# Kernel optimization log

Measured on AMD Instinct MI355X. Metric: run time of the kernel, lower is better.

Reference implementation:

```python
import jax, jax.numpy as jnp
import numpy as np

EMBED = 256
HEADS = 8
HD = EMBED // HEADS
LEVELS = 4
POINTS = 4
FFN_H = 1024
BS = 8
LQ = 900
SHAPES = [(100, 100), (50, 50), (25, 25), (13, 13)]


def setup_inputs() -> dict:
    key = jax.random.key(0)
    ks = jax.random.split(key, 20)
    nv = sum(h * w for h, w in SHAPES)
    starts = np.cumsum([0] + [h * w for h, w in SHAPES])[:-1]
    inp = {
        "queries": jax.random.normal(ks[0], (BS, LQ, EMBED), jnp.float32),
        "memory": jax.random.normal(ks[1], (BS, nv, EMBED), jnp.float32),
        "query_pos": jax.random.normal(ks[2], (BS, LQ, EMBED), jnp.float32),
        "reference_points": jax.random.uniform(ks[3], (BS, LQ, LEVELS, 4), jnp.float32) * 0.9 + 0.05,
        "spatial_shapes": jnp.asarray(SHAPES, jnp.int32),
        "level_start_index": jnp.asarray(starts, jnp.int32),
    }
    def lin(k, din, dout):
        k1, k2 = jax.random.split(k)
        w = jax.random.normal(k1, (din, dout), jnp.float32) * 0.02
        b = jax.random.normal(k2, (dout,), jnp.float32) * 0.01
        return w, b
    specs = [("Wq", "bq", EMBED, EMBED), ("Wk", "bk", EMBED, EMBED), ("Wv", "bv", EMBED, EMBED),
             ("Wo", "bo", EMBED, EMBED), ("Wvd", "bvd", EMBED, EMBED),
             ("Woff", "boff", EMBED, HEADS * LEVELS * POINTS * 2),
             ("Watt", "batt", EMBED, HEADS * LEVELS * POINTS),
             ("Wop", "bop", EMBED, EMBED), ("Wg", "bg", 2 * EMBED, 2 * EMBED),
             ("W1", "b1", EMBED, FFN_H), ("W2", "b2", FFN_H, EMBED)]
    for i, (wn, bn, di, do) in enumerate(specs):
        w, b = lin(ks[4 + i], di, do)
        inp[wn] = w
        inp[bn] = b
    for n in ["ln1", "ln2", "ln3"]:
        inp[n + "_s"] = jnp.ones((EMBED,), jnp.float32)
        inp[n + "_b"] = jnp.zeros((EMBED,), jnp.float32)
    return inp


def _ln(x, s, b):
    m = jnp.mean(x, -1, keepdims=True)
    v = jnp.mean(jnp.square(x - m), -1, keepdims=True)
    return (x - m) * jax.lax.rsqrt(v + 1e-5) * s + b


def _bilinear(v_l, lx, ly, H, W):
    # v_l: [bs,h,H*W,hd]; lx,ly: [bs,h,lq,p] normalized in [0,1]
    # grid_sample(align_corners=False, padding=zeros) semantics
    px = lx * W - 0.5
    py = ly * H - 0.5
    x0 = jnp.floor(px)
    y0 = jnp.floor(py)
    wx = px - x0
    wy = py - y0
    x0i = x0.astype(jnp.int32)
    y0i = y0.astype(jnp.int32)
    bs, h, lq, p = lx.shape
    out = jnp.zeros((bs, h, lq, p, HD), v_l.dtype)
    for dy in (0, 1):
        for dx in (0, 1):
            xi = x0i + dx
            yi = y0i + dy
            w = (wx if dx else 1.0 - wx) * (wy if dy else 1.0 - wy)
            valid = (xi >= 0) & (xi < W) & (yi >= 0) & (yi < H)
            idx = jnp.clip(yi, 0, H - 1) * W + jnp.clip(xi, 0, W - 1)
            g = jnp.take_along_axis(v_l, idx.reshape(bs, h, lq * p)[..., None], axis=2)
            g = g.reshape(bs, h, lq, p, HD)
            out = out + w[..., None] * jnp.where(valid[..., None], g, 0.0)
    return out


def reference(queries, memory, query_pos, reference_points, spatial_shapes, level_start_index,
              Wq, bq, Wk, bk, Wv, bv, Wo, bo, Wvd, bvd, Woff, boff, Watt, batt, Wop, bop,
              Wg, bg, W1, b1, W2, b2, ln1_s, ln1_b, ln2_s, ln2_b, ln3_s, ln3_b):
    bs, lq, _ = queries.shape
    shp = np.asarray(spatial_shapes)
    st = np.asarray(level_start_index)

    # ---- self attention (pre-norm, q=k=x+pos, v=x) ----
    x = _ln(queries, ln1_s, ln1_b)
    qk = x + query_pos
    Q = (qk @ Wq + bq).reshape(bs, lq, HEADS, HD)
    K = (qk @ Wk + bk).reshape(bs, lq, HEADS, HD)
    V = (x @ Wv + bv).reshape(bs, lq, HEADS, HD)
    scores = jnp.einsum('bqhd,bkhd->bhqk', Q, K) * (1.0 / np.sqrt(HD))
    attn = jax.nn.softmax(scores, axis=-1)
    sa = jnp.einsum('bhqk,bkhd->bqhd', attn, V).reshape(bs, lq, EMBED) @ Wo + bo
    x1 = queries + sa  # dropout is identity in eval

    # ---- MS-deformable cross attention ----
    y = _ln(x1, ln2_s, ln2_b)
    qc = y + query_pos
    val = (memory @ Wvd + bvd).reshape(bs, -1, HEADS, HD).transpose(0, 2, 1, 3)  # [bs,h,Nv,hd]
    off = (qc @ Woff + boff).reshape(bs, lq, HEADS, LEVELS, POINTS, 2)
    aw = jax.nn.softmax((qc @ Watt + batt).reshape(bs, lq, HEADS, LEVELS * POINTS), axis=-1)
    aw = aw.reshape(bs, lq, HEADS, LEVELS, POINTS)
    rp = reference_points[:, :, None, :, None, :]  # [bs,lq,1,L,1,4]
    loc = rp[..., :2] + off / POINTS * rp[..., 2:] * 0.5  # [bs,lq,h,L,p,2]

    out = jnp.zeros((bs, HEADS, lq, HD), queries.dtype)
    for l in range(LEVELS):
        H, W = int(shp[l, 0]), int(shp[l, 1])
        s0 = int(st[l])
        v_l = val[:, :, s0:s0 + H * W]
        lx = jnp.transpose(loc[:, :, :, l, :, 0], (0, 2, 1, 3))  # [bs,h,lq,p]
        ly = jnp.transpose(loc[:, :, :, l, :, 1], (0, 2, 1, 3))
        samp = _bilinear(v_l, lx, ly, H, W)  # [bs,h,lq,p,hd]
        w = jnp.transpose(aw[:, :, :, l], (0, 2, 1, 3))  # [bs,h,lq,p]
        out = out + jnp.sum(w[..., None] * samp, axis=3)
    cross = out.transpose(0, 2, 1, 3).reshape(bs, lq, EMBED) @ Wop + bop

    # ---- gated fusion ----
    gi = jnp.concatenate([x1, cross], axis=-1)
    g = jax.nn.sigmoid(gi @ Wg + bg)
    x2 = g[..., :EMBED] * x1 + g[..., EMBED:] * cross

    # ---- FFN ----
    z = _ln(x2, ln3_s, ln3_b)
    ffn = jax.nn.relu(z @ W1 + b1) @ W2 + b2
    return (x2 + ffn, aw, loc)
```

## Files before the change

kernel.cpp:

```cpp
#include <hip/hip_runtime.h>
#include <hip/hip_bf16.h>
#include <math.h>

#define BB 8
#define LQ 900
#define EE 256
#define NH 8
#define HD 32
#define NL 4
#define NP 4
#define FFN_H 1024

typedef __bf16 bf16x8 __attribute__((ext_vector_type(8)));
typedef float f32x4 __attribute__((ext_vector_type(4)));
typedef unsigned short u16x8 __attribute__((ext_vector_type(8)));

__device__ __forceinline__ unsigned short f2b(float f) {
    union { float f; unsigned int u; } v; v.f = f;
    unsigned int u = v.u;
    unsigned int r = (u + 0x7fffu + ((u >> 16) & 1u)) >> 16;
    return (unsigned short)r;
}
__device__ __forceinline__ float b2f(unsigned short h) {
    union { unsigned int u; float f; } v; v.u = ((unsigned int)h) << 16; return v.f;
}

typedef __attribute__((address_space(3))) unsigned int* lds_ptr_t;
typedef const __attribute__((address_space(1))) unsigned int* gbl_ptr_t;
#define GLOAD16(g, l) __builtin_amdgcn_global_load_lds((gbl_ptr_t)(g), (lds_ptr_t)(l), 16, 0, 0)
#define VMCNT(n) asm volatile("s_waitcnt vmcnt(" #n ")" ::: "memory")
#define LGKM0()  asm volatile("s_waitcnt lgkmcnt(0)" ::: "memory")

struct TDesc { const float* src; unsigned short* dst; int K, N, tile0; };
struct TPack {
    TDesc d[11];
    const float *bq, *bk, *boff, *batt;
    float *bqk, *boa;
};

__global__ __launch_bounds__(256) void prep_kernel(
    TPack p,
    const float* __restrict__ queries, const float* __restrict__ qpos,
    const float* __restrict__ ln1_s, const float* __restrict__ ln1_b,
    unsigned short* __restrict__ x_b, unsigned short* __restrict__ qk_b)
{
    const int bi = blockIdx.x;
    const int t = threadIdx.x;

    if (bi < 1248) {
        int di = 0;
#pragma unroll
        for (int i = 1; i < 11; ++i) if (bi >= p.d[i].tile0) di = i;
        TDesc d = p.d[di];
        int tt = bi - d.tile0;
        int tn = (d.N + 31) >> 5;
        int tk = tt / tn, tc = tt % tn;
        __shared__ float tile[32][33];
        int tx = t & 31, ty = t >> 5;
#pragma unroll
        for (int i = 0; i < 4; ++i) {
            int kk = tk * 32 + ty + i * 8, nn = tc * 32 + tx;
            tile[ty + i * 8][tx] = d.src[(size_t)kk * d.N + nn];
        }
        __syncthreads();
#pragma unroll
        for (int i = 0; i < 4; ++i) {
            int nn = tc * 32 + ty + i * 8, kk = tk * 32 + tx;
            d.dst[(size_t)nn * d.K + kk] = f2b(tile[tx][ty + i * 8]);
        }
        return;
    }
    if (bi < 1252) {
        int which = bi - 1248;
        if (which == 0)      p.bqk[t] = p.bq[t];
        else if (which == 1) p.bqk[256 + t] = p.bk[t];
        else if (which == 2) p.boa[t] = p.boff[t];
        else if (t < 128)    p.boa[256 + t] = p.batt[t];
        return;
    }
    {
        const int row = bi - 1252;
        const int w = t >> 6, lane = t & 63;
        __shared__ float red[4];
        float v = queries[(size_t)row * EE + t];
        float sum = v;
#pragma unroll
        for (int o = 32; o; o >>= 1) sum += __shfl_xor(sum, o, 64);
        if (lane == 0) red[w] = sum;
        __syncthreads();
        float mean = (red[0] + red[1] + red[2] + red[3]) * (1.0f / 256.0f);
        __syncthreads();
        float dd = v - mean;
        float sq = dd * dd;
#pragma unroll
        for (int o = 32; o; o >>= 1) sq += __shfl_xor(sq, o, 64);
        if (lane == 0) red[w] = sq;
        __syncthreads();
        float var = (red[0] + red[1] + red[2] + red[3]) * (1.0f / 256.0f);
        float y = dd * rsqrtf(var + 1e-5f) * ln1_s[t] + ln1_b[t];
        x_b[(size_t)row * EE + t]  = f2b(y);
        qk_b[(size_t)row * EE + t] = f2b(y + qpos[(size_t)row * EE + t]);
    }
}

struct GD {
    const unsigned short* A;
    const float* Af;
    const unsigned short* Bt;
    const float* bias;
    const float* resid;
    float* outF;
    unsigned short* outB;
    const float* lnS; const float* lnB; const float* lnAdd;
    unsigned short* lnOut;
    int M, K, N, ntN, tile0, ldOutB, outBoff, act, aF32;
};
struct GB { GD d[3]; int nd, tot; };

template<int BN>
__global__ __launch_bounds__(256, (BN == 128) ? 4 : 2) void gemm_pipe(GB g) {
    __shared__ __align__(16) unsigned short ldsb[2][(64 + BN) * 32];
    __shared__ float lnred[2][64][2];
    const int tid = threadIdx.x;
    const int l = tid & 63, w = tid >> 6;
    const int wr = w >> 1, wc = w & 1;
    constexpr int NJ = BN / 32;

    int t = blockIdx.x;
    if (t >= g.tot) return;
    int d = 0;
    while (d + 1 < g.nd && t >= g.d[d + 1].tile0) ++d;

    const int sc = tid & 3;
    float4 fA[2];

    auto stage = [&](int dd, int tt, int ks, int pp) {
        const GD& D = g.d[dd];
        int local = tt - D.tile0;
        int m0 = (local / D.ntN) * 64;
        int n0 = (local % D.ntN) * BN;
        unsigned short* base = &ldsb[pp][0];
        if (D.aF32) {
            int row = tid >> 2;
            int rg = m0 + row; int mm = D.M - 1; rg = rg < mm ? rg : mm;
            int ck = (sc ^ ((row >> 1) & 3)) * 8;
            const float* src = D.Af + (size_t)rg * D.K + (ks << 5) + ck;
            fA[0] = *(const float4*)src;
            fA[1] = *(const float4*)(src + 4);
        } else {
            int row = w * 16 + (l >> 2);
            int rg = m0 + row; int mm = D.M - 1; rg = rg < mm ? rg : mm;
            int schunk = ((l & 3) ^ ((row >> 1) & 3)) << 4;
            GLOAD16((const char*)(D.A + (size_t)rg * D.K + (ks << 5)) + schunk,
                    base + (w * 16) * 32);
        }
#pragma unroll
        for (int ib = 0; ib < BN / 64; ++ib) {
            int row = ib * 64 + w * 16 + (l >> 2);
            int rg = n0 + row; int nn = D.N - 1; rg = rg < nn ? rg : nn;
            int schunk = ((l & 3) ^ ((row >> 1) & 3)) << 4;
            GLOAD16((const char*)(D.Bt + (size_t)rg * D.K + (ks << 5)) + schunk,
                    base + 2048 + (ib * 64 + w * 16) * 32);
        }
    };
    auto commitA = [&](int pp) {
        int row = tid >> 2;
        u16x8 o;
        o[0] = f2b(fA[0].x); o[1] = f2b(fA[0].y); o[2] = f2b(fA[0].z); o[3] = f2b(fA[0].w);
        o[4] = f2b(fA[1].x); o[5] = f2b(fA[1].y); o[6] = f2b(fA[1].z); o[7] = f2b(fA[1].w);
        *(u16x8*)((char*)&ldsb[pp][0] + row * 64 + sc * 16) = o;
    };

    stage(d, t, 0, 0);
    if (g.d[d].aF32) { commitA(0); LGKM0(); }
    int p = 0;

    while (true) {
        const GD D = g.d[d];
        int local = t - D.tile0;
        const int m0 = (local / D.ntN) * 64;
        const int n0 = (local % D.ntN) * BN;
        const int nk = D.K >> 5;

        f32x4 acc[2][NJ];
#pragma unroll
        for (int i = 0; i < 2; ++i)
#pragma unroll
            for (int j = 0; j < NJ; ++j) acc[i][j] = (f32x4){0.f, 0.f, 0.f, 0.f};

        for (int ks = 0; ks < nk; ++ks) {
            int nt = t, nks = ks + 1, ndd = d;
            bool have = true;
            if (nks == nk) {
                nt = t + gridDim.x; nks = 0;
                if (nt >= g.tot) have = false;
                else { while (ndd + 1 < g.nd && nt >= g.d[ndd + 1].tile0) ++ndd; }
            }
            bool stagedAF = have && g.d[ndd].aF32;
            if (have) {
                stage(ndd, nt, nks, p ^ 1);
                if (stagedAF) {
                    if constexpr (BN == 128) { VMCNT(4); } else { VMCNT(6); }
                } else {
                    if constexpr (BN == 128) { VMCNT(3); } else { VMCNT(5); }
                }
            } else {
                VMCNT(0);
            }
            __builtin_amdgcn_sched_barrier(0);
            __builtin_amdgcn_s_barrier();
            __builtin_amdgcn_sched_barrier(0);
            {
                const char* base = (const char*)&ldsb[p][0];
                const int rch = ((l >> 4) ^ ((l >> 1) & 3)) << 4;
                bf16x8 af[2];
#pragma unroll
                for (int i = 0; i < 2; ++i) {
                    int row = wr * 32 + i * 16 + (l & 15);
                    af[i] = *(const bf16x8*)(base + row * 64 + rch);
                }
#pragma unroll
                for (int j = 0; j < NJ; ++j) {
                    int row = wc * (BN / 2) + j * 16 + (l & 15);
                    bf16x8 bfr = *(const bf16x8*)(base + 4096 + row * 64 + rch);
#pragma unroll
                    for (int i = 0; i < 2; ++i)
                        acc[i][j] = __builtin_amdgcn_mfma_f32_16x16x32_bf16(af[i], bfr, acc[i][j], 0, 0, 0);
                }
            }
            if (stagedAF) { commitA(p ^ 1); LGKM0(); }
            __builtin_amdgcn_sched_barrier(0);
            __builtin_amdgcn_s_barrier();
            __builtin_amdgcn_sched_barrier(0);
            p ^= 1;
        }

#pragma unroll
        for (int i = 0; i < 2; ++i) {
#pragma unroll
            for (int r = 0; r < 4; ++r) {
                int gm = m0 + wr * 32 + i * 16 + ((l >> 4) << 2) + r;
                if (gm >= D.M) continue;
#pragma unroll
                for (int j = 0; j < NJ; ++j) {
                    int gn = n0 + wc * (BN / 2) + j * 16 + (l & 15);
                    if (gn >= D.N) continue;
                    float v = acc[i][j][r];
                    if (D.bias)  v += D.bias[gn];
                    if (D.resid) v += D.resid[(size_t)gm * D.N + gn];
                    if (D.act == 1)      v = fmaxf(v, 0.f);
                    else if (D.act == 2) v = 1.0f / (1.0f + __expf(-v));
                    acc[i][j][r] = v;
                    if (D.outF) D.outF[(size_t)gm * D.N + gn] = v;
                    if (D.outB) D.outB[(size_t)gm * D.ldOutB + D.outBoff + gn] = f2b(v);
                }
            }
        }

        if constexpr (BN == 256) {
            if (D.lnOut) {
#pragma unroll
                for (int i = 0; i < 2; ++i) {
#pragma unroll
                    for (int r = 0; r < 4; ++r) {
                        float s1 = 0.f, s2 = 0.f;
#pragma unroll
                        for (int j = 0; j < NJ; ++j) {
                            float v = acc[i][j][r];
                            s1 += v; s2 += v * v;
                        }
#pragma unroll
                        for (int o = 1; o <= 8; o <<= 1) {
                            s1 += __shfl_xor(s1, o, 64);
                            s2 += __shfl_xor(s2, o, 64);
                        }
                        if ((l & 15) == 0) {
                            int row = wr * 32 + i * 16 + ((l >> 4) << 2) + r;
                            lnred[wc][row][0] = s1;
                            lnred[wc][row][1] = s2;
                        }
                    }
                }
                __syncthreads();
#pragma unroll
                for (int i = 0; i < 2; ++i) {
#pragma unroll
                    for (int r = 0; r < 4; ++r) {
                        int row = wr * 32 + i * 16 + ((l >> 4) << 2) + r;
                        int gm = m0 + row;
                        if (gm >= D.M) continue;
                        float mean = (lnred[0][row][0] + lnred[1][row][0]) * (1.0f / 256.0f);
                        float msq  = (lnred[0][row][1] + lnred[1][row][1]) * (1.0f / 256.0f);
                        float rs = rsqrtf(msq - mean * mean + 1e-5f);
#pragma unroll
                        for (int j = 0; j < NJ; ++j) {
                            int gn = wc * (BN / 2) + j * 16 + (l & 15);
                            float y = (acc[i][j][r] - mean) * rs * D.lnS[gn] + D.lnB[gn]
                                      + D.lnAdd[(size_t)gm * 256 + gn];
                            D.lnOut[(size_t)gm * 256 + gn] = f2b(y);
                        }
                    }
                }
            }
        }

        t += gridDim.x;
        if (t >= g.tot) break;
        while (d + 1 < g.nd && t >= g.d[d + 1].tile0) ++d;
    }
}

__global__ __launch_bounds__(256) void attn_mfma(
    const unsigned short* __restrict__ QK, const unsigned short* __restrict__ Vb,
    unsigned short* __restrict__ outB)
{
    const int qt = blockIdx.x;
    const int bh = blockIdx.y;
    const int b = bh >> 3, h = bh & 7;
    const int tid = threadIdx.x;
    const int w = tid >> 6, l = tid & 63;

    __shared__ __align__(16) unsigned short Ks[64 * 32];
    __shared__ __align__(16) unsigned short VT[32 * 64];
    __shared__ __align__(16) unsigned short Ps[4][64 * 20];

    const int qrow_w = qt * 64 + w * 16;
    int qr = qrow_w + (l & 15); qr = qr < LQ ? qr : LQ - 1;
    bf16x8 qf = *(const bf16x8*)(QK + ((size_t)(b * LQ + qr)) * 512 + h * 32 + (l >> 4) * 8);

    f32x4 acc0 = {0.f, 0.f, 0.f, 0.f}, acc1 = {0.f, 0.f, 0.f, 0.f};
    float m_run = -1e30f, l_run = 0.f;
    const float scale = 0.17677669529663689f;
    const f32x4 z4 = {0.f, 0.f, 0.f, 0.f};

    const int key = tid >> 2;
    const int dg = (tid & 3) * 8;
    u16x8 kvc, vvc, kvn, vvn;
    {
        int krow = key; krow = krow < LQ ? krow : LQ - 1;
        size_t base = (size_t)(b * LQ + krow);
        kvc = *(const u16x8*)(QK + base * 512 + 256 + h * 32 + dg);
        vvc = *(const u16x8*)(Vb + base * 256 + h * 32 + dg);
    }

    for (int kt = 0; kt < 15; ++kt) {
        __syncthreads();
        *(u16x8*)((char*)Ks + key * 64 + ((dg * 2) ^ ((key & 3) << 4))) = kvc;
#pragma unroll
        for (int e = 0; e < 8; ++e) {
            int dd = dg + e;
            *(unsigned short*)((char*)VT + dd * 128 + ((key * 2) ^ ((dd & 7) << 4))) = vvc[e];
        }
        if (kt < 14) {
            int krow = (kt + 1) * 64 + key; krow = krow < LQ ? krow : LQ - 1;
            size_t base = (size_t)(b * LQ + krow);
            kvn = *(const u16x8*)(QK + base * 512 + 256 + h * 32 + dg);
            vvn = *(const u16x8*)(Vb + base * 256 + h * 32 + dg);
        }
        __syncthreads();

        float p[4][4];
        float tmax = -1e30f;
#pragma unroll
        for (int m = 0; m < 4; ++m) {
            int kr = m * 16 + (l & 15);
            bf16x8 kf = *(const bf16x8*)((const char*)Ks + kr * 64 +
                        (((l >> 4) * 16) ^ ((kr & 3) << 4)));
            f32x4 sf = __builtin_amdgcn_mfma_f32_16x16x32_bf16(kf, qf, z4, 0, 0, 0);
#pragma unroll
            for (int r = 0; r < 4; ++r) {
                int kk = kt * 64 + m * 16 + (l >> 4) * 4 + r;
                float sv = (kk < LQ) ? sf[r] * scale : -1e30f;
                p[m][r] = sv;
                tmax = fmaxf(tmax, sv);
            }
        }
        tmax = fmaxf(tmax, __shfl_xor(tmax, 16, 64));
        tmax = fmaxf(tmax, __shfl_xor(tmax, 32, 64));
        float newm = fmaxf(m_run, tmax);
        float corr = __expf(m_run - newm);
        m_run = newm;
        float tsum = 0.f;
#pragma unroll
        for (int m = 0; m < 4; ++m)
#pragma unroll
            for (int r = 0; r < 4; ++r) {
                float e = __expf(p[m][r] - newm);
                p[m][r] = e;
                tsum += e;
            }
        tsum += __shfl_xor(tsum, 16, 64);
        tsum += __shfl_xor(tsum, 32, 64);
        l_run = l_run * corr + tsum;
        acc0 *= corr;
        acc1 *= corr;

        unsigned short* pw = &Ps[w][0];
#pragma unroll
        for (int m = 0; m < 4; ++m)
#pragma unroll
            for (int r = 0; r < 4; ++r) {
                int kk = m * 16 + (l >> 4) * 4 + r;
                pw[kk * 20 + (l & 15)] = f2b(p[m][r]);
            }

#pragma unroll
        for (int s = 0; s < 2; ++s) {
            union { unsigned short u[8]; bf16x8 v; } pb;
#pragma unroll
            for (int j = 0; j < 8; ++j)
                pb.u[j] = pw[(s * 32 + (l >> 4) * 8 + j) * 20 + (l & 15)];
#pragma unroll
            for (int m2 = 0; m2 < 2; ++m2) {
                int dd = m2 * 16 + (l & 15);
                bf16x8 vf = *(const bf16x8*)((const char*)VT + dd * 128 +
                            ((s * 64 + (l >> 4) * 16) ^ ((dd & 7) << 4)));
                if (m2 == 0) acc0 = __builtin_amdgcn_mfma_f32_16x16x32_bf16(vf, pb.v, acc0, 0, 0, 0);
                else         acc1 = __builtin_amdgcn_mfma_f32_16x16x32_bf16(vf, pb.v, acc1, 0, 0, 0);
            }
        }
        if (kt < 14) { kvc = kvn; vvc = vvn; }
    }

    float inv = 1.0f / l_run;
    int q = qrow_w + (l & 15);
    if (q < LQ) {
        size_t obase = ((size_t)(b * LQ + q)) * 256 + h * 32;
#pragma unroll
        for (int r = 0; r < 4; ++r) {
            int d0 = (l >> 4) * 4 + r;
            outB[obase + d0]      = f2b(acc0[r] * inv);
            outB[obase + 16 + d0] = f2b(acc1[r] * inv);
        }
    }
}

__global__ __launch_bounds__(256) void sample_fused(
    const float* __restrict__ off_att, const float* __restrict__ refp,
    const unsigned short* __restrict__ val,
    const int* __restrict__ shapes, const int* __restrict__ starts,
    float* __restrict__ aw_out, float* __restrict__ loc_out,
    unsigned short* __restrict__ samp, int NV)
{
    const int row = blockIdx.x;
    const int b = row / LQ;
    const int t = threadIdx.x;
    const int h = t >> 5, d = t & 31;

    __shared__ float l_logit[128];
    __shared__ float l_aw[128];
    __shared__ float l_loc[256];
    __shared__ int l_sh[NL * 2];
    __shared__ int l_st[NL];

    if (t < 128) l_logit[t] = off_att[(size_t)row * 384 + 256 + t];
    {
        float o = off_att[(size_t)row * 384 + t];
        int c = t & 1;
        int lv = (t >> 3) & 3;
        float rc = refp[((size_t)row * 4 + lv) * 4 + c];
        float rs = refp[((size_t)row * 4 + lv) * 4 + 2 + c];
        float loc = rc + o * 0.125f * rs;
        l_loc[t] = loc;
        loc_out[(size_t)row * 256 + t] = loc;
    }
    if (t < NL * 2) l_sh[t] = shapes[t];
    if (t < NL) l_st[t] = starts[t];
    __syncthreads();
    if (t < 128) {
        int hh = t >> 4;
        float mx = -1e30f;
#pragma unroll
        for (int i = 0; i < 16; ++i) mx = fmaxf(mx, l_logit[hh * 16 + i]);
        float sum = 0.f;
#pragma unroll
        for (int i = 0; i < 16; ++i) sum += __expf(l_logit[hh * 16 + i] - mx);
        float aw = __expf(l_logit[t] - mx) / sum;
        l_aw[t] = aw;
        aw_out[(size_t)row * 128 + t] = aw;
    }
    __syncthreads();

    float acc = 0.f;
    const unsigned short* vb = val + (size_t)b * NV * EE + h * HD + d;

#pragma unroll
    for (int lv = 0; lv < NL; ++lv) {
        const int Hh = l_sh[lv * 2], Ww = l_sh[lv * 2 + 1];
        const int s0 = l_st[lv];
#pragma unroll
        for (int p = 0; p < NP; ++p) {
            const int base = ((h * NL + lv) * NP + p) * 2;
            float lx = l_loc[base], ly = l_loc[base + 1];
            float wgt0 = l_aw[h * 16 + lv * NP + p];
            float px = lx * (float)Ww - 0.5f;
            float py = ly * (float)Hh - 0.5f;
            float x0f = floorf(px), y0f = floorf(py);
            float wx = px - x0f, wy = py - y0f;
            int x0 = (int)x0f, y0 = (int)y0f;
#pragma unroll
            for (int dy = 0; dy < 2; ++dy) {
                int yi = y0 + dy;
                bool vy = (yi >= 0) && (yi < Hh);
                int yc = min(max(yi, 0), Hh - 1);
                float wyv = dy ? wy : 1.f - wy;
#pragma unroll
                for (int dx = 0; dx < 2; ++dx) {
                    int xi = x0 + dx;
                    bool vv = vy && (xi >= 0) && (xi < Ww);
                    int xc = min(max(xi, 0), Ww - 1);
                    float wgt = wgt0 * wyv * (dx ? wx : 1.f - wx);
                    float gv = b2f(vb[(size_t)(s0 + yc * Ww + xc) * EE]);
                    acc += vv ? wgt * gv : 0.f;
                }
            }
        }
    }
    samp[(size_t)row * EE + t] = f2b(acc);
}

__global__ __launch_bounds__(256) void gate_ln3(
    const float* __restrict__ g, const float* __restrict__ x1,
    const float* __restrict__ cross, const float* __restrict__ s,
    const float* __restrict__ bln, float* __restrict__ x2out,
    unsigned short* __restrict__ zb)
{
    const int row = blockIdx.x;
    const int t = threadIdx.x;
    const int w = t >> 6;
    const int lane = t & 63;
    __shared__ float red[4];

    float g1 = g[(size_t)row * 512 + t];
    float g2 = g[(size_t)row * 512 + 256 + t];
    float v = g1 * x1[(size_t)row * EE + t] + g2 * cross[(size_t)row * EE + t];
    x2out[(size_t)row * EE + t] = v;

    float sum = v;
#pragma unroll
    for (int o = 32; o; o >>= 1) sum += __shfl_xor(sum, o, 64);
    if (lane == 0) red[w] = sum;
    __syncthreads();
    float mean = (red[0] + red[1] + red[2] + red[3]) * (1.0f / 256.0f);
    __syncthreads();

    float d = v - mean;
    float sq = d * d;
#pragma unroll
    for (int o = 32; o; o >>= 1) sq += __shfl_xor(sq, o, 64);
    if (lane == 0) red[w] = sq;
    __syncthreads();
    float var = (red[0] + red[1] + red[2] + red[3]) * (1.0f / 256.0f);

    float y = d * rsqrtf(var + 1e-5f) * s[t] + bln[t];
    zb[(size_t)row * EE + t] = f2b(y);
}

extern "C" void kernel_launch(void* const* d_in, const int* in_sizes, int n_in,
                              void* d_out, int out_size, void* d_ws, size_t ws_size,
                              hipStream_t stream)
{
    const float* queries   = (const float*)d_in[0];
    const float* memory    = (const float*)d_in[1];
    const float* query_pos = (const float*)d_in[2];
    const float* refp      = (const float*)d_in[3];
    const int*   shapes    = (const int*)d_in[4];
    const int*   starts    = (const int*)d_in[5];
    const float* Wq  = (const float*)d_in[6],  *bq  = (const float*)d_in[7];
    const float* Wk  = (const float*)d_in[8],  *bk  = (const float*)d_in[9];
    const float* Wv  = (const float*)d_in[10], *bv  = (const float*)d_in[11];
    const float* Wo  = (const float*)d_in[12], *bo  = (const float*)d_in[13];
    const float* Wvd = (const float*)d_in[14], *bvd = (const float*)d_in[15];
    const float* Woff= (const float*)d_in[16], *boff= (const float*)d_in[17];
    const float* Watt= (const float*)d_in[18], *batt= (const float*)d_in[19];
    const float* Wop = (const float*)d_in[20], *bop = (const float*)d_in[21];
    const float* Wg  = (const float*)d_in[22], *bg  = (const float*)d_in[23];
    const float* W1  = (const float*)d_in[24], *b1  = (const float*)d_in[25];
    const float* W2  = (const float*)d_in[26], *b2  = (const float*)d_in[27];
    const float* ln1_s = (const float*)d_in[28], *ln1_b = (const float*)d_in[29];
    const float* ln2_s = (const float*)d_in[30], *ln2_b = (const float*)d_in[31];
    const float* ln3_s = (const float*)d_in[32], *ln3_b = (const float*)d_in[33];

    const int NV = in_sizes[1] / (BB * EE);
    const int Mq = BB * LQ;
    const int Mv = BB * NV;
    const long memN = (long)Mv * EE;

    char* W8 = (char*)d_ws;
    size_t off = 0;
    auto alloc = [&](size_t bytes) { char* p = W8 + off; off += (bytes + 255) & ~(size_t)255; return p; };

    unsigned short* val_b = (unsigned short*)alloc((size_t)memN * 2);
    unsigned short* WtQK  = (unsigned short*)alloc(512 * 256 * 2);
    unsigned short* WtV   = (unsigned short*)alloc(256 * 256 * 2);
    unsigned short* WtO   = (unsigned short*)alloc(256 * 256 * 2);
    unsigned short* WtVD  = (unsigned short*)alloc(256 * 256 * 2);
    unsigned short* WtOA  = (unsigned short*)alloc(384 * 256 * 2);
    unsigned short* WtOP  = (unsigned short*)alloc(256 * 256 * 2);
    unsigned short* WtG   = (unsigned short*)alloc(512 * 512 * 2);
    unsigned short* Wt1   = (unsigned short*)alloc(1024 * 256 * 2);
    unsigned short* Wt2   = (unsigned short*)alloc(256 * 1024 * 2);
    float*          bqk   = (float*)alloc(512 * 4);
    float*          boa   = (float*)alloc(384 * 4);
    unsigned short* qkb   = (unsigned short*)alloc((size_t)Mq * 512 * 2);
    unsigned short* vb_buf= (unsigned short*)alloc((size_t)Mq * 256 * 2);
    unsigned short* av_buf= (unsigned short*)alloc((size_t)Mq * 256 * 2);
    float*          x1    = (float*)alloc((size_t)Mq * 256 * 4);
    unsigned short* xc_cat= (unsigned short*)alloc((size_t)Mq * 512 * 2);
    unsigned short* qc_b  = (unsigned short*)alloc((size_t)Mq * 256 * 2);
    unsigned short* qk_b  = (unsigned short*)alloc((size_t)Mq * 256 * 2);
    float*          cross = (float*)alloc((size_t)Mq * 256 * 4);

    unsigned short* x_b = (unsigned short*)cross;
    float* off_att = (float*)qkb;
    unsigned short* samp_b = av_buf;
    float* gbuf = (float*)val_b;
    float* x2   = (float*)((char*)val_b + (size_t)Mq * 512 * 4);
    unsigned short* z_b = (unsigned short*)((char*)x2 + (size_t)Mq * 256 * 4);
    unsigned short* hidden_b = (unsigned short*)((char*)z_b + (size_t)Mq * 256 * 2);

    float* out0    = (float*)d_out;
    float* aw_out  = out0 + (size_t)Mq * 256;
    float* loc_out = aw_out + (size_t)Mq * 128;

    dim3 blk(256);
    const int tMq = (Mq + 63) / 64;
    const int tv  = (Mv + 63) / 64;

    TPack tp;
    tp.d[0]  = { Wq,   WtQK,             256, 256,    0 };
    tp.d[1]  = { Wk,   WtQK + 256 * 256, 256, 256,   64 };
    tp.d[2]  = { Wv,   WtV,              256, 256,  128 };
    tp.d[3]  = { Wo,   WtO,              256, 256,  192 };
    tp.d[4]  = { Wvd,  WtVD,             256, 256,  256 };
    tp.d[5]  = { Woff, WtOA,             256, 256,  320 };
    tp.d[6]  = { Watt, WtOA + 256 * 256, 256, 128,  384 };
    tp.d[7]  = { Wop,  WtOP,             256, 256,  416 };
    tp.d[8]  = { Wg,   WtG,              512, 512,  480 };
    tp.d[9]  = { W1,   Wt1,              256, 1024, 736 };
    tp.d[10] = { W2,   Wt2,             1024, 256,  992 };
    tp.bq = bq; tp.bk = bk; tp.boff = boff; tp.batt = batt;
    tp.bqk = bqk; tp.boa = boa;
    prep_kernel<<<1252 + Mq, blk, 0, stream>>>(
        tp, queries, query_pos, ln1_s, ln1_b, x_b, qk_b);

    {
        GB g; g.nd = 3;
        g.d[0] = { nullptr, memory, WtVD, bvd, nullptr, nullptr, val_b,
                   nullptr, nullptr, nullptr, nullptr,
                   Mv, 256, 256, 2, 0, 256, 0, 0, 1 };
        g.d[1] = { qk_b, nullptr, WtQK, bqk, nullptr, nullptr, qkb,
                   nullptr, nullptr, nullptr, nullptr,
                   Mq, 256, 512, 4, tv * 2, 512, 0, 0, 0 };
        g.d[2] = { x_b, nullptr, WtV, bv, nullptr, nullptr, vb_buf,
                   nullptr, nullptr, nullptr, nullptr,
                   Mq, 256, 256, 2, tv * 2 + tMq * 4, 256, 0, 0, 0 };
        g.tot = tv * 2 + tMq * 6;
        gemm_pipe<128><<<1536, blk, 0, stream>>>(g);
    }

    attn_mfma<<<dim3(15, BB * NH), blk, 0, stream>>>(qkb, vb_buf, av_buf);

    {
        GB g; g.nd = 1;
        g.d[0] = { av_buf, nullptr, WtO, bo, queries, x1, xc_cat,
                   ln2_s, ln2_b, query_pos, qc_b,
                   Mq, 256, 256, 1, 0, 512, 0, 0, 0 };
        g.tot = tMq;
        gemm_pipe<256><<<tMq, blk, 0, stream>>>(g);
    }

    {
        GB g; g.nd = 1;
        g.d[0] = { qc_b, nullptr, WtOA, boa, nullptr, off_att, nullptr,
                   nullptr, nullptr, nullptr, nullptr,
                   Mq, 256, 384, 3, 0, 384, 0, 0, 0 };
        g.tot = tMq * 3;
        gemm_pipe<128><<<g.tot, blk, 0, stream>>>(g);
    }

    sample_fused<<<Mq, blk, 0, stream>>>(off_att, refp, val_b, shapes, starts,
                                         aw_out, loc_out, samp_b, NV);

    {
        GB g; g.nd = 1;
        g.d[0] = { samp_b, nullptr, WtOP, bop, nullptr, cross, xc_cat,
                   nullptr, nullptr, nullptr, nullptr,
                   Mq, 256, 256, 2, 0, 512, 256, 0, 0 };
        g.tot = tMq * 2;
        gemm_pipe<128><<<g.tot, blk, 0, stream>>>(g);
    }

    {
        GB g; g.nd = 1;
        g.d[0] = { xc_cat, nullptr, WtG, bg, nullptr, gbuf, nullptr,
                   nullptr, nullptr, nullptr, nullptr,
                   Mq, 512, 512, 4, 0, 512, 0, 2, 0 };
        g.tot = tMq * 4;
        gemm_pipe<128><<<g.tot, blk, 0, stream>>>(g);
    }

    gate_ln3<<<Mq, blk, 0, stream>>>(gbuf, x1, cross, ln3_s, ln3_b, x2, z_b);

    {
        GB g; g.nd = 1;
        g.d[0] = { z_b, nullptr, Wt1, b1, nullptr, nullptr, hidden_b,
                   nullptr, nullptr, nullptr, nullptr,
                   Mq, 256, 1024, 8, 0, 1024, 0, 1, 0 };
        g.tot = tMq * 8;
        gemm_pipe<128><<<g.tot, blk, 0, stream>>>(g);
    }

    {
        GB g; g.nd = 1;
        g.d[0] = { hidden_b, nullptr, Wt2, b2, x2, out0, nullptr,
                   nullptr, nullptr, nullptr, nullptr,
                   Mq, 1024, 256, 2, 0, 256, 0, 0, 0 };
        g.tot = tMq * 2;
        gemm_pipe<128><<<g.tot, blk, 0, stream>>>(g);
    }
}
```

Baseline: 333.5 us.

## Fold Wop into gate weights and batch cross/gate GEMMs; pre-convert memory to bf16

Folds the output projection Wop into the second half of the gate weight matrix (Wop·Wg_bottom, plus a folded bias), so the gate GEMM can consume the sampled features directly. The cross projection and the gate GEMM then run in a single batched launch instead of two dependent launches. Memory is also converted to bf16 inside the prep kernel so the value-projection GEMM uses the async LDS load path instead of fp32 loads with per-tile conversion. In exchange, prep gains a naive 256-long dot loop per weight column and an extra full pass over memory, and the folded weights are rounded to bf16 after the product, which slightly changes numerics.

```diff
diff --git a/kernel.cpp b/kernel.cpp
--- a/kernel.cpp
+++ b/kernel.cpp
@@ -33,24 +33,28 @@
 
 struct TDesc { const float* src; unsigned short* dst; int K, N, tile0; };
 struct TPack {
-    TDesc d[11];
+    TDesc d[10];
     const float *bq, *bk, *boff, *batt;
     float *bqk, *boa;
+    const float *Wg_src, *Wop_src, *bop_src, *bg_src;
+    unsigned short* WtGF;
+    float* bgg;
 };
 
 __global__ __launch_bounds__(256) void prep_kernel(
     TPack p,
     const float* __restrict__ queries, const float* __restrict__ qpos,
     const float* __restrict__ ln1_s, const float* __restrict__ ln1_b,
-    unsigned short* __restrict__ x_b, unsigned short* __restrict__ qk_b)
+    unsigned short* __restrict__ x_b, unsigned short* __restrict__ qk_b,
+    const float* __restrict__ mem, unsigned short* __restrict__ mem_b, long memN)
 {
     const int bi = blockIdx.x;
     const int t = threadIdx.x;
 
-    if (bi < 1248) {
+    if (bi < 992) {
         int di = 0;
 #pragma unroll
-        for (int i = 1; i < 11; ++i) if (bi >= p.d[i].tile0) di = i;
+        for (int i = 1; i < 10; ++i) if (bi >= p.d[i].tile0) di = i;
         TDesc d = p.d[di];
         int tt = bi - d.tile0;
         int tn = (d.N + 31) >> 5;
@@ -70,16 +74,16 @@
         }
         return;
     }
-    if (bi < 1252) {
-        int which = bi - 1248;
+    if (bi < 996) {
+        int which = bi - 992;
         if (which == 0)      p.bqk[t] = p.bq[t];
         else if (which == 1) p.bqk[256 + t] = p.bk[t];
         else if (which == 2) p.boa[t] = p.boff[t];
         else if (t < 128)    p.boa[256 + t] = p.batt[t];
         return;
     }
-    {
-        const int row = bi - 1252;
+    if (bi < 8196) {
+        const int row = bi - 996;
         const int w = t >> 6, lane = t & 63;
         __shared__ float red[4];
         float v = queries[(size_t)row * EE + t];
@@ -100,6 +104,36 @@
         float y = dd * rsqrtf(var + 1e-5f) * ln1_s[t] + ln1_b[t];
         x_b[(size_t)row * EE + t]  = f2b(y);
         qk_b[(size_t)row * EE + t] = f2b(y + qpos[(size_t)row * EE + t]);
+        return;
+    }
+    if (bi < 10244) {
+        long i = ((long)(bi - 8196) * 256 + t) * 8;
+        long stride = (long)2048 * 256 * 8;
+        for (; i < memN; i += stride) {
+            float4 a = *(const float4*)(mem + i);
+            float4 b = *(const float4*)(mem + i + 4);
+            u16x8 o;
+            o[0] = f2b(a.x); o[1] = f2b(a.y); o[2] = f2b(a.z); o[3] = f2b(a.w);
+            o[4] = f2b(b.x); o[5] = f2b(b.y); o[6] = f2b(b.z); o[7] = f2b(b.w);
+            *(u16x8*)(mem_b + i) = o;
+        }
+        return;
+    }
+    {
+        const int n = bi - 10244;
+        __shared__ float wgcol[256];
+        wgcol[t] = p.Wg_src[(size_t)(256 + t) * 512 + n];
+        __syncthreads();
+        p.WtGF[(size_t)n * 512 + t] = f2b(p.Wg_src[(size_t)t * 512 + n]);
+        float dot = 0.f;
+        for (int j = 0; j < 256; ++j)
+            dot += p.Wop_src[(size_t)t * 256 + j] * wgcol[j];
+        p.WtGF[(size_t)n * 512 + 256 + t] = f2b(dot);
+        if (t == 0) {
+            float bb = p.bg_src[n];
+            for (int j = 0; j < 256; ++j) bb += p.bop_src[j] * wgcol[j];
+            p.bgg[n] = bb;
+        }
     }
 }
 
@@ -113,7 +147,7 @@
     unsigned short* outB;
     const float* lnS; const float* lnB; const float* lnAdd;
     unsigned short* lnOut;
-    int M, K, N, ntN, tile0, ldOutB, outBoff, act, aF32;
+    int M, K, N, ntN, tile0, ldOutB, outBoff, act, aF32, ldA;
 };
 struct GB { GD d[3]; int nd, tot; };
 
@@ -136,6 +170,7 @@
 
     auto stage = [&](int dd, int tt, int ks, int pp) {
         const GD& D = g.d[dd];
+        const int lda = D.ldA ? D.ldA : D.K;
         int local = tt - D.tile0;
         int m0 = (local / D.ntN) * 64;
         int n0 = (local % D.ntN) * BN;
@@ -144,14 +179,14 @@
             int row = tid >> 2;
             int rg = m0 + row; int mm = D.M - 1; rg = rg < mm ? rg : mm;
             int ck = (sc ^ ((row >> 1) & 3)) * 8;
-            const float* src = D.Af + (size_t)rg * D.K + (ks << 5) + ck;
+            const float* src = D.Af + (size_t)rg * lda + (ks << 5) + ck;
             fA[0] = *(const float4*)src;
             fA[1] = *(const float4*)(src + 4);
         } else {
             int row = w * 16 + (l >> 2);
             int rg = m0 + row; int mm = D.M - 1; rg = rg < mm ? rg : mm;
             int schunk = ((l & 3) ^ ((row >> 1) & 3)) << 4;
-            GLOAD16((const char*)(D.A + (size_t)rg * D.K + (ks << 5)) + schunk,
+            GLOAD16((const char*)(D.A + (size_t)rg * lda + (ks << 5)) + schunk,
                     base + (w * 16) * 32);
         }
 #pragma unroll
@@ -440,7 +475,7 @@
     const unsigned short* __restrict__ val,
     const int* __restrict__ shapes, const int* __restrict__ starts,
     float* __restrict__ aw_out, float* __restrict__ loc_out,
-    unsigned short* __restrict__ samp, int NV)
+    unsigned short* __restrict__ xs, int NV)
 {
     const int row = blockIdx.x;
     const int b = row / LQ;
@@ -516,7 +551,7 @@
             }
         }
     }
-    samp[(size_t)row * EE + t] = f2b(acc);
+    xs[(size_t)row * 512 + 256 + t] = f2b(acc);
 }
 
 __global__ __launch_bounds__(256) void gate_ln3(
@@ -590,6 +625,7 @@
     size_t off = 0;
     auto alloc = [&](size_t bytes) { char* p = W8 + off; off += (bytes + 255) & ~(size_t)255; return p; };
 
+    unsigned short* mem_b = (unsigned short*)alloc((size_t)memN * 2);
     unsigned short* val_b = (unsigned short*)alloc((size_t)memN * 2);
     unsigned short* WtQK  = (unsigned short*)alloc(512 * 256 * 2);
     unsigned short* WtV   = (unsigned short*)alloc(256 * 256 * 2);
@@ -597,25 +633,25 @@
     unsigned short* WtVD  = (unsigned short*)alloc(256 * 256 * 2);
     unsigned short* WtOA  = (unsigned short*)alloc(384 * 256 * 2);
     unsigned short* WtOP  = (unsigned short*)alloc(256 * 256 * 2);
-    unsigned short* WtG   = (unsigned short*)alloc(512 * 512 * 2);
+    unsigned short* WtGF  = (unsigned short*)alloc(512 * 512 * 2);
     unsigned short* Wt1   = (unsigned short*)alloc(1024 * 256 * 2);
     unsigned short* Wt2   = (unsigned short*)alloc(256 * 1024 * 2);
     float*          bqk   = (float*)alloc(512 * 4);
     float*          boa   = (float*)alloc(384 * 4);
+    float*          bgg   = (float*)alloc(512 * 4);
     unsigned short* qkb   = (unsigned short*)alloc((size_t)Mq * 512 * 2);
     unsigned short* vb_buf= (unsigned short*)alloc((size_t)Mq * 256 * 2);
     unsigned short* av_buf= (unsigned short*)alloc((size_t)Mq * 256 * 2);
     float*          x1    = (float*)alloc((size_t)Mq * 256 * 4);
-    unsigned short* xc_cat= (unsigned short*)alloc((size_t)Mq * 512 * 2);
+    unsigned short* xs_cat= (unsigned short*)alloc((size_t)Mq * 512 * 2);
     unsigned short* qc_b  = (unsigned short*)alloc((size_t)Mq * 256 * 2);
     unsigned short* qk_b  = (unsigned short*)alloc((size_t)Mq * 256 * 2);
     float*          cross = (float*)alloc((size_t)Mq * 256 * 4);
 
     unsigned short* x_b = (unsigned short*)cross;
     float* off_att = (float*)qkb;
-    unsigned short* samp_b = av_buf;
-    float* gbuf = (float*)val_b;
-    float* x2   = (float*)((char*)val_b + (size_t)Mq * 512 * 4);
+    float* gbuf = (float*)mem_b;
+    float* x2   = (float*)((char*)mem_b + (size_t)Mq * 512 * 4);
     unsigned short* z_b = (unsigned short*)((char*)x2 + (size_t)Mq * 256 * 4);
     unsigned short* hidden_b = (unsigned short*)((char*)z_b + (size_t)Mq * 256 * 2);
 
@@ -628,27 +664,28 @@
     const int tv  = (Mv + 63) / 64;
 
     TPack tp;
-    tp.d[0]  = { Wq,   WtQK,             256, 256,    0 };
-    tp.d[1]  = { Wk,   WtQK + 256 * 256, 256, 256,   64 };
-    tp.d[2]  = { Wv,   WtV,              256, 256,  128 };
-    tp.d[3]  = { Wo,   WtO,              256, 256,  192 };
-    tp.d[4]  = { Wvd,  WtVD,             256, 256,  256 };
-    tp.d[5]  = { Woff, WtOA,             256, 256,  320 };
-    tp.d[6]  = { Watt, WtOA + 256 * 256, 256, 128,  384 };
-    tp.d[7]  = { Wop,  WtOP,             256, 256,  416 };
-    tp.d[8]  = { Wg,   WtG,              512, 512,  480 };
-    tp.d[9]  = { W1,   Wt1,              256, 1024, 736 };
-    tp.d[10] = { W2,   Wt2,             1024, 256,  992 };
+    tp.d[0] = { Wq,   WtQK,             256, 256,    0 };
+    tp.d[1] = { Wk,   WtQK + 256 * 256, 256, 256,   64 };
+    tp.d[2] = { Wv,   WtV,              256, 256,  128 };
+    tp.d[3] = { Wo,   WtO,              256, 256,  192 };
+    tp.d[4] = { Wvd,  WtVD,             256, 256,  256 };
+    tp.d[5] = { Woff, WtOA,             256, 256,  320 };
+    tp.d[6] = { Watt, WtOA + 256 * 256, 256, 128,  384 };
+    tp.d[7] = { Wop,  WtOP,             256, 256,  416 };
+    tp.d[8] = { W1,   Wt1,              256, 1024, 480 };
+    tp.d[9] = { W2,   Wt2,             1024, 256,  736 };
     tp.bq = bq; tp.bk = bk; tp.boff = boff; tp.batt = batt;
     tp.bqk = bqk; tp.boa = boa;
-    prep_kernel<<<1252 + Mq, blk, 0, stream>>>(
-        tp, queries, query_pos, ln1_s, ln1_b, x_b, qk_b);
+    tp.Wg_src = Wg; tp.Wop_src = Wop; tp.bop_src = bop; tp.bg_src = bg;
+    tp.WtGF = WtGF; tp.bgg = bgg;
+    prep_kernel<<<10756, blk, 0, stream>>>(
+        tp, queries, query_pos, ln1_s, ln1_b, x_b, qk_b, memory, mem_b, memN);
 
     {
         GB g; g.nd = 3;
-        g.d[0] = { nullptr, memory, WtVD, bvd, nullptr, nullptr, val_b,
+        g.d[0] = { mem_b, nullptr, WtVD, bvd, nullptr, nullptr, val_b,
                    nullptr, nullptr, nullptr, nullptr,
-                   Mv, 256, 256, 2, 0, 256, 0, 0, 1 };
+                   Mv, 256, 256, 2, 0, 256, 0, 0, 0 };
         g.d[1] = { qk_b, nullptr, WtQK, bqk, nullptr, nullptr, qkb,
                    nullptr, nullptr, nullptr, nullptr,
                    Mq, 256, 512, 4, tv * 2, 512, 0, 0, 0 };
@@ -663,7 +700,7 @@
 
     {
         GB g; g.nd = 1;
-        g.d[0] = { av_buf, nullptr, WtO, bo, queries, x1, xc_cat,
+        g.d[0] = { av_buf, nullptr, WtO, bo, queries, x1, xs_cat,
                    ln2_s, ln2_b, query_pos, qc_b,
                    Mq, 256, 256, 1, 0, 512, 0, 0, 0 };
         g.tot = tMq;
@@ -680,23 +717,17 @@
     }
 
     sample_fused<<<Mq, blk, 0, stream>>>(off_att, refp, val_b, shapes, starts,
-                                         aw_out, loc_out, samp_b, NV);
-
-    {
-        GB g; g.nd = 1;
-        g.d[0] = { samp_b, nullptr, WtOP, bop, nullptr, cross, xc_cat,
+                                         aw_out, loc_out, xs_cat, NV);
+
+    {
+        GB g; g.nd = 2;
+        g.d[0] = { xs_cat + 256, nullptr, WtOP, bop, nullptr, cross, nullptr,
                    nullptr, nullptr, nullptr, nullptr,
-                   Mq, 256, 256, 2, 0, 512, 256, 0, 0 };
-        g.tot = tMq * 2;
-        gemm_pipe<128><<<g.tot, blk, 0, stream>>>(g);
-    }
-
-    {
-        GB g; g.nd = 1;
-        g.d[0] = { xc_cat, nullptr, WtG, bg, nullptr, gbuf, nullptr,
+                   Mq, 256, 256, 2, 0, 0, 0, 0, 0, 512 };
+        g.d[1] = { xs_cat, nullptr, WtGF, bgg, nullptr, gbuf, nullptr,
                    nullptr, nullptr, nullptr, nullptr,
-                   Mq, 512, 512, 4, 0, 512, 0, 2, 0 };
-        g.tot = tMq * 4;
+                   Mq, 512, 512, 4, tMq * 2, 0, 0, 2, 0, 0 };
+        g.tot = tMq * 6;
         gemm_pipe<128><<<g.tot, blk, 0, stream>>>(g);
     }
 
```

Measured after the change: 360.2 us. 1.08x slower.
